# Performance work log

Measured on AMD Instinct MI355X. Metric: run time of the kernel, lower is better.

## Reference

```python
import jax, jax.numpy as jnp
import numpy as np

B, N, DIM = 2, 2048, 1024
HEADS, DH, NUM_MEM = 8, 64, 4
EPS = 1e-5


def layer_norm(x, gamma):
    mu = x.mean(-1, keepdims=True)
    var = ((x - mu) ** 2).mean(-1, keepdims=True)
    return (x - mu) * jax.lax.rsqrt(var + EPS) * gamma


def setup_inputs() -> dict:
    key = jax.random.key(0)
    ks = jax.random.split(key, 7)
    x = jax.random.normal(ks[0], (B, N, DIM), jnp.float32)
    mask = jax.random.randint(ks[1], (B, N), 0, 2) > 0
    attn_bias = jax.random.normal(ks[2], (HEADS, N, N), jnp.float32) * 0.02
    gamma = jnp.ones((DIM,), jnp.float32)
    Wq = jax.random.normal(ks[3], (DIM, HEADS * DH), jnp.float32) * (DIM ** -0.5)
    Wkv = jax.random.normal(ks[4], (DIM, 2 * DH), jnp.float32) * (DIM ** -0.5)
    mem_kv = jax.random.normal(ks[5], (2, NUM_MEM, DH), jnp.float32)
    Wout = jax.random.normal(ks[6], (HEADS * DH, DIM), jnp.float32) * ((HEADS * DH) ** -0.5)
    return dict(x=x, attn_bias=attn_bias, gamma=gamma, Wq=Wq, Wkv=Wkv,
                mem_kv=mem_kv, Wout=Wout, mask=mask)


def reference(x, attn_bias, gamma, Wq, Wkv, mem_kv, Wout, mask):
    b, n, _ = x.shape
    # norm applied to query path only; kv comes from pre-norm x (self-attention)
    xn = layer_norm(x, gamma)
    q = (xn @ Wq).reshape(b, n, HEADS, DH).transpose(0, 2, 1, 3) * (DH ** -0.5)  # b h n d
    kv = x @ Wkv  # multi-query: single shared kv head
    k, v = kv[..., :DH], kv[..., DH:]
    mk = jnp.broadcast_to(mem_kv[0], (b, NUM_MEM, DH))
    mv = jnp.broadcast_to(mem_kv[1], (b, NUM_MEM, DH))
    k = jnp.concatenate([mk, k], axis=1)  # b (m+n) d
    v = jnp.concatenate([mv, v], axis=1)
    j = n + NUM_MEM
    bias = jnp.pad(attn_bias, ((0, 0), (0, 0), (NUM_MEM, 0)))  # zero bias on mem tokens
    maskp = jnp.pad(mask, ((0, 0), (NUM_MEM, 0)), constant_values=True)
    sim = jnp.einsum('bhid,bjd->bhij', q, k) + bias
    neg = -jnp.finfo(sim.dtype).max
    sim = jnp.where(maskp[:, None, None, :], sim, neg)
    causal = jnp.triu(jnp.ones((n, j), bool), k=NUM_MEM + 1)  # mem tokens always visible
    sim = jnp.where(causal, neg, sim)
    attn = jax.nn.softmax(sim, axis=-1)
    out = jnp.einsum('bhij,bjd->bhid', attn, v)
    out = out.transpose(0, 2, 1, 3).reshape(b, n, HEADS * DH)
    return out @ Wout
```

## Files before the change

### kernel.cpp

```cpp
#include <hip/hip_runtime.h>
#include <hip/hip_bf16.h>
#include <float.h>

#define B_ 2
#define N_ 2048
#define DIM_ 1024
#define HEADS_ 8
#define DH_ 64
#define NUM_MEM_ 4
#define ROWS_ (B_ * N_)
#define QCOLS_ (HEADS_ * DH_)
#define JTOT_ (N_ + NUM_MEM_)
#define JPAD_ 2176
#define CHUNKS_PER_BH_ 77

typedef __attribute__((ext_vector_type(8))) short short8v;
typedef __attribute__((ext_vector_type(4))) float f32x4;

static __device__ __forceinline__ ushort f2b(float f) {
    __hip_bfloat16 hb = __float2bfloat16(f);
    return *(ushort*)&hb;
}
static __device__ __forceinline__ uint pk2(float a, float b) {
    return ((uint)f2b(b) << 16) | (uint)f2b(a);
}
static __device__ __forceinline__ float b2f_lo(uint u) {
    union { uint x; float f; } c; c.x = u << 16; return c.f;
}
static __device__ __forceinline__ float b2f_hi(uint u) {
    union { uint x; float f; } c; c.x = u & 0xffff0000u; return c.f;
}

__global__ __launch_bounds__(256) void ln_cast_kernel(const float* __restrict__ x,
                                                      const float* __restrict__ gamma,
                                                      ushort* __restrict__ xb,
                                                      ushort* __restrict__ xnb) {
    int row = blockIdx.x;
    const float4 v = ((const float4*)(x + (size_t)row * DIM_))[threadIdx.x];
    float s  = v.x + v.y + v.z + v.w;
    float s2 = v.x * v.x + v.y * v.y + v.z * v.z + v.w * v.w;
    #pragma unroll
    for (int off = 32; off > 0; off >>= 1) {
        s  += __shfl_down(s, off);
        s2 += __shfl_down(s2, off);
    }
    __shared__ float ws1[4], ws2[4];
    int lane = threadIdx.x & 63, wid = threadIdx.x >> 6;
    if (lane == 0) { ws1[wid] = s; ws2[wid] = s2; }
    __syncthreads();
    float tot  = ws1[0] + ws1[1] + ws1[2] + ws1[3];
    float tot2 = ws2[0] + ws2[1] + ws2[2] + ws2[3];
    float mu  = tot * (1.0f / DIM_);
    float var = tot2 * (1.0f / DIM_) - mu * mu;
    float rs  = rsqrtf(var + 1e-5f);
    const float4 g = ((const float4*)gamma)[threadIdx.x];
    float vv[4] = {v.x, v.y, v.z, v.w};
    float gg[4] = {g.x, g.y, g.z, g.w};
    ushort xo[4], xno[4];
    #pragma unroll
    for (int j = 0; j < 4; ++j) {
        xo[j]  = f2b(vv[j]);
        xno[j] = f2b((vv[j] - mu) * rs * gg[j]);
    }
    *(int2*)(xb  + (size_t)row * DIM_ + threadIdx.x * 4) = *(int2*)xo;
    *(int2*)(xnb + (size_t)row * DIM_ + threadIdx.x * 4) = *(int2*)xno;
}

static __device__ __forceinline__ void wtrans_body(const float* __restrict__ W,
                                                   ushort* __restrict__ Wt,
                                                   int K, int N, int t) {
    int n = t % N;
    int k0 = (t / N) * 8;
    ushort u[8];
    #pragma unroll
    for (int j = 0; j < 8; ++j) u[j] = f2b(W[(size_t)(k0 + j) * N + n]);
    *(int4*)(Wt + (size_t)n * K + k0) = *(int4*)u;
}

__global__ __launch_bounds__(256) void prep_kernel(const float* __restrict__ Wq,
                                                   const float* __restrict__ Wkv,
                                                   const float* __restrict__ Wout,
                                                   const float* __restrict__ mem_kv,
                                                   const int* __restrict__ mask,
                                                   ushort* __restrict__ Wqt,
                                                   ushort* __restrict__ Wkvt,
                                                   ushort* __restrict__ Woutt,
                                                   ushort* __restrict__ Kb,
                                                   ushort* __restrict__ Vt,
                                                   ushort* __restrict__ amask) {
    int bid = blockIdx.x;
    int tid = threadIdx.x;
    if (bid < 256) {
        wtrans_body(Wq, Wqt, DIM_, QCOLS_, bid * 256 + tid);
    } else if (bid < 320) {
        wtrans_body(Wkv, Wkvt, DIM_, 2 * DH_, (bid - 256) * 256 + tid);
    } else if (bid < 576) {
        wtrans_body(Wout, Woutt, QCOLS_, DIM_, (bid - 320) * 256 + tid);
    } else if (bid < 640) {
        int t = (bid - 576) * 256 + tid;
        int d  = t & 63;
        int ji = (t >> 6) & 127;
        int b  = t >> 13;
        int j  = (ji < NUM_MEM_) ? ji : (2048 + ji);
        float kv_ = 0.f, vv = 0.f;
        if (ji < NUM_MEM_) {
            kv_ = mem_kv[ji * DH_ + d];
            vv  = mem_kv[NUM_MEM_ * DH_ + ji * DH_ + d];
        }
        Kb[((size_t)(b * JPAD_) + j) * DH_ + d] = f2b(kv_);
        Vt[((size_t)(b * DH_) + d) * JPAD_ + j] = f2b(vv);
    } else {
        int t = (bid - 640) * 256 + tid;
        if (t < B_ * JPAD_) {
            int b = t / JPAD_;
            int j = t % JPAD_;
            float v;
            if (j < NUM_MEM_) v = 0.f;
            else if (j < JTOT_) v = mask[b * N_ + (j - NUM_MEM_)] ? 0.f : -1e30f;
            else v = -1e30f;
            amask[(size_t)b * JPAD_ + j] = f2b(v);
        }
    }
}

template<int MODE, int BM>
__global__ __launch_bounds__(256) void gemm_bf16(const ushort* __restrict__ A,
                                                 const ushort* __restrict__ Bt,
                                                 void* __restrict__ C,
                                                 void* __restrict__ C2,
                                                 int M, int N, int K) {
    constexpr int RT = BM / 64;
    __shared__ ushort As[BM][40];
    __shared__ ushort Bs[64][40];
    int tid = threadIdx.x;
    int w = tid >> 6, l = tid & 63, lg = l >> 4, ll = l & 15;
    int r0 = blockIdx.y * BM, c0 = blockIdx.x * 64;

    int arow = tid >> 2;
    int achk = (tid & 3) * 8;
    const ushort* Ap  = A + (size_t)(r0 + arow) * K + achk;
    const ushort* Ap2 = Ap + (size_t)64 * K;
    const ushort* Bp  = Bt + (size_t)(c0 + arow) * K + achk;

    int4 a0 = *(const int4*)Ap;
    int4 a1;
    if constexpr (RT == 2) a1 = *(const int4*)Ap2;
    int4 b0 = *(const int4*)Bp;

    f32x4 acc[RT][4] = {};

    int nk = K / 32;
    for (int ks = 0; ks < nk; ++ks) {
        __syncthreads();
        *(int4*)&As[arow][achk] = a0;
        if constexpr (RT == 2) *(int4*)&As[arow + 64][achk] = a1;
        *(int4*)&Bs[arow][achk] = b0;
        __syncthreads();
        int kn = (ks + 1 < nk) ? (ks + 1) * 32 : 0;
        a0 = *(const int4*)(Ap + kn);
        if constexpr (RT == 2) a1 = *(const int4*)(Ap2 + kn);
        b0 = *(const int4*)(Bp + kn);
        short8v af[RT], bf[4];
        #pragma unroll
        for (int rt = 0; rt < RT; ++rt)
            af[rt] = *(const short8v*)&As[w * 16 * RT + rt * 16 + ll][lg * 8];
        #pragma unroll
        for (int ct = 0; ct < 4; ++ct)
            bf[ct] = *(const short8v*)&Bs[ct * 16 + ll][lg * 8];
        __builtin_amdgcn_s_setprio(1);
        #pragma unroll
        for (int rt = 0; rt < RT; ++rt)
            #pragma unroll
            for (int ct = 0; ct < 4; ++ct)
                acc[rt][ct] = __builtin_amdgcn_mfma_f32_16x16x32_bf16(af[rt], bf[ct], acc[rt][ct], 0, 0, 0);
        __builtin_amdgcn_s_setprio(0);
    }

    #pragma unroll
    for (int rt = 0; rt < RT; ++rt) {
        #pragma unroll
        for (int ct = 0; ct < 4; ++ct) {
            #pragma unroll
            for (int r = 0; r < 4; ++r) {
                int row = r0 + w * 16 * RT + rt * 16 + lg * 4 + r;
                int col = c0 + ct * 16 + ll;
                float val = acc[rt][ct][r];
                if (MODE == 0) {
                    ((ushort*)C)[(size_t)row * QCOLS_ + col] = f2b(val * 0.125f);
                } else if (MODE == 1) {
                    int b = row >> 11;
                    int j = (row & 2047) + NUM_MEM_;
                    if (col < DH_)
                        ((ushort*)C)[((size_t)(b * JPAD_) + j) * DH_ + col] = f2b(val);
                    else
                        ((ushort*)C2)[((size_t)(b * DH_) + (col - DH_)) * JPAD_ + j] = f2b(val);
                } else {
                    ((float*)C)[(size_t)row * DIM_ + col] = val;
                }
            }
        }
    }
}

__global__ __launch_bounds__(256, 4) void fattn_split_kernel(const ushort* __restrict__ qb,
                                                             const ushort* __restrict__ Kb,
                                                             const ushort* __restrict__ Vt,
                                                             const float* __restrict__ bias,
                                                             const ushort* __restrict__ amask,
                                                             float* __restrict__ part_O,
                                                             float* __restrict__ part_ml) {
    __shared__ ushort Ks[64][72];
    __shared__ ushort Vs[64][72];
    __shared__ ushort Pt[4][16][72];

    int cid = blockIdx.x;
    int bh  = cid / CHUNKS_PER_BH_;
    int rem = cid - bh * CHUNKS_PER_BH_;
    int b = bh >> 3, h = bh & 7;
    int qt = 0, ci = 0;
    {
        int cum = 0;
        #pragma unroll 1
        for (int t = 0; t < 32; ++t) {
            int c = (t + 10) / 9;
            if (rem < cum + c) { qt = t; ci = rem - cum; break; }
            cum += c;
        }
    }
    int nt = qt + 2;
    int nc = (qt + 10) / 9;
    int t0 = ci * nt / nc;
    int t1 = (ci + 1) * nt / nc;
    int q0 = qt * 64;

    int tid = threadIdx.x;
    int w  = tid >> 6;
    int l  = tid & 63;
    int lg = l >> 4;
    int ll = l & 15;
    int i_row = q0 + w * 16 + ll;

    short8v aq0, aq1;
    {
        const ushort* qp = qb + ((size_t)(b * N_ + i_row)) * QCOLS_ + h * DH_;
        aq0 = *(const short8v*)(qp + lg * 8);
        aq1 = *(const short8v*)(qp + 32 + lg * 8);
    }

    const float*  bias_row = bias + ((size_t)h * N_ + i_row) * N_;
    const ushort* am_row   = amask + (size_t)b * JPAD_;

    int sr = tid >> 3, sc = (tid & 7) * 8;
    const ushort* KbB = Kb + (size_t)b * JPAD_ * DH_;
    const ushort* VtB = Vt + (size_t)b * DH_ * JPAD_;

    int jp0 = t0 * 64;
    int4 kr0 = *(const int4*)(KbB + (size_t)(jp0 + sr) * DH_ + sc);
    int4 kr1 = *(const int4*)(KbB + (size_t)(jp0 + sr + 32) * DH_ + sc);
    int4 vr0 = *(const int4*)(VtB + (size_t)sr * JPAD_ + jp0 + sc);
    int4 vr1 = *(const int4*)(VtB + (size_t)(sr + 32) * JPAD_ + jp0 + sc);

    f32x4 oacc[4] = {};
    float mrow1 = -1e30f, lsum1 = 0.f;

    for (int jt = t0; jt < t1; ++jt) {
        int j0 = jt * 64;
        __syncthreads();
        *(int4*)&Ks[sr][sc]      = kr0;
        *(int4*)&Ks[sr + 32][sc] = kr1;
        *(int4*)&Vs[sr][sc]      = vr0;
        *(int4*)&Vs[sr + 32][sc] = vr1;
        __syncthreads();

        float4 bb[4];
        uint2  am[4];
        #pragma unroll
        for (int ct = 0; ct < 4; ++ct) {
            int js = j0 + ct * 16 + lg * 4;
            int sj = js - NUM_MEM_;
            int sjc = sj < 0 ? 0 : (sj > N_ - 4 ? N_ - 4 : sj);
            bb[ct] = *(const float4*)(bias_row + sjc);
            am[ct] = *(const uint2*)(am_row + js);
        }

        int jn0 = (jt + 1 < t1 ? jt + 1 : jt) * 64;
        kr0 = *(const int4*)(KbB + (size_t)(jn0 + sr) * DH_ + sc);
        kr1 = *(const int4*)(KbB + (size_t)(jn0 + sr + 32) * DH_ + sc);
        vr0 = *(const int4*)(VtB + (size_t)sr * JPAD_ + jn0 + sc);
        vr1 = *(const int4*)(VtB + (size_t)(sr + 32) * JPAD_ + jn0 + sc);

        float s[4][4];
        #pragma unroll
        for (int ct = 0; ct < 4; ++ct) {
            f32x4 acc = {};
            short8v bk0 = *(const short8v*)&Ks[ct * 16 + ll][lg * 8];
            short8v bk1 = *(const short8v*)&Ks[ct * 16 + ll][32 + lg * 8];
            __builtin_amdgcn_s_setprio(1);
            acc = __builtin_amdgcn_mfma_f32_16x16x32_bf16(bk0, aq0, acc, 0, 0, 0);
            acc = __builtin_amdgcn_mfma_f32_16x16x32_bf16(bk1, aq1, acc, 0, 0, 0);
            __builtin_amdgcn_s_setprio(0);
            float amf[4] = { b2f_lo(am[ct].x), b2f_hi(am[ct].x),
                             b2f_lo(am[ct].y), b2f_hi(am[ct].y) };
            #pragma unroll
            for (int r = 0; r < 4; ++r)
                s[ct][r] = acc[r] + bb[ct][r] + amf[r];
            if (ct == 0 && jt == 0) {
                #pragma unroll
                for (int r = 0; r < 4; ++r)
                    if (lg == 0) s[0][r] = acc[r];
            }
        }
        if (jt >= qt) {
            #pragma unroll
            for (int ct = 0; ct < 4; ++ct)
                #pragma unroll
                for (int r = 0; r < 4; ++r) {
                    int js = j0 + ct * 16 + lg * 4 + r;
                    s[ct][r] = (js <= i_row + NUM_MEM_) ? s[ct][r] : -1e30f;
                }
        }

        float m01 = fmaxf(fmaxf(s[0][0], s[0][1]), fmaxf(s[0][2], s[0][3]));
        float m23 = fmaxf(fmaxf(s[1][0], s[1][1]), fmaxf(s[1][2], s[1][3]));
        float m45 = fmaxf(fmaxf(s[2][0], s[2][1]), fmaxf(s[2][2], s[2][3]));
        float m67 = fmaxf(fmaxf(s[3][0], s[3][1]), fmaxf(s[3][2], s[3][3]));
        float m = fmaxf(fmaxf(m01, m23), fmaxf(m45, m67));
        m = fmaxf(m, __shfl_xor(m, 16));
        m = fmaxf(m, __shfl_xor(m, 32));
        float mn = fmaxf(mrow1, m);
        float scl = __expf(mrow1 - mn);
        mrow1 = mn;

        float ps = 0.f;
        #pragma unroll
        for (int ct = 0; ct < 4; ++ct)
            #pragma unroll
            for (int r = 0; r < 4; ++r) {
                float p = __expf(s[ct][r] - mn);
                s[ct][r] = p;
                ps += p;
            }
        ps += __shfl_xor(ps, 16);
        ps += __shfl_xor(ps, 32);
        lsum1 = lsum1 * scl + ps;

        #pragma unroll
        for (int ct = 0; ct < 4; ++ct) {
            uint2 pu;
            pu.x = pk2(s[ct][0], s[ct][1]);
            pu.y = pk2(s[ct][2], s[ct][3]);
            *(uint2*)&Pt[w][ll][ct * 16 + lg * 4] = pu;
        }
        #pragma unroll
        for (int dt = 0; dt < 4; ++dt)
            #pragma unroll
            for (int r = 0; r < 4; ++r) oacc[dt][r] *= scl;

        #pragma unroll
        for (int c = 0; c < 2; ++c) {
            short8v ptf = *(const short8v*)&Pt[w][ll][c * 32 + lg * 8];
            __builtin_amdgcn_s_setprio(1);
            #pragma unroll
            for (int dt = 0; dt < 4; ++dt) {
                short8v bv = *(const short8v*)&Vs[dt * 16 + ll][c * 32 + lg * 8];
                oacc[dt] = __builtin_amdgcn_mfma_f32_16x16x32_bf16(bv, ptf, oacc[dt], 0, 0, 0);
            }
            __builtin_amdgcn_s_setprio(0);
        }
    }

    int slot = (bh * 32 + qt) * 4 + ci;
    float* po = part_O + (size_t)slot * 4096;
    #pragma unroll
    for (int dt = 0; dt < 4; ++dt)
        *(f32x4*)&po[(w * 16 + ll) * 64 + dt * 16 + lg * 4] = oacc[dt];
    if (lg == 0) {
        part_ml[(size_t)slot * 128 + (w * 16 + ll) * 2]     = mrow1;
        part_ml[(size_t)slot * 128 + (w * 16 + ll) * 2 + 1] = lsum1;
    }
}

__global__ __launch_bounds__(256) void merge_kernel(const float* __restrict__ part_O,
                                                    const float* __restrict__ part_ml,
                                                    ushort* __restrict__ attn_ob) {
    int bid = blockIdx.x;
    int qt = bid & 31;
    int bh = bid >> 5;
    int b = bh >> 3, h = bh & 7;
    int nc = (qt + 10) / 9;
    int tid = threadIdx.x;
    int row = tid >> 2;
    int dseg = (tid & 3) * 16;
    int slot0 = bid * 4;

    float M = -1e30f;
    #pragma unroll
    for (int c = 0; c < 4; ++c) {
        if (c >= nc) break;
        M = fmaxf(M, part_ml[(size_t)(slot0 + c) * 128 + row * 2]);
    }
    float den = 0.f;
    float num[16] = {};
    #pragma unroll
    for (int c = 0; c < 4; ++c) {
        if (c >= nc) break;
        float m_c = part_ml[(size_t)(slot0 + c) * 128 + row * 2];
        float l_c = part_ml[(size_t)(slot0 + c) * 128 + row * 2 + 1];
        float wgt = __expf(m_c - M);
        den += wgt * l_c;
        const float4* src = (const float4*)(part_O + (size_t)(slot0 + c) * 4096 + row * 64 + dseg);
        #pragma unroll
        for (int e = 0; e < 4; ++e) {
            float4 v = src[e];
            num[e * 4 + 0] += wgt * v.x;
            num[e * 4 + 1] += wgt * v.y;
            num[e * 4 + 2] += wgt * v.z;
            num[e * 4 + 3] += wgt * v.w;
        }
    }
    float inv = 1.f / den;
    ushort o[16];
    #pragma unroll
    for (int e = 0; e < 16; ++e) o[e] = f2b(num[e] * inv);
    int i = qt * 64 + row;
    ushort* dst = attn_ob + ((size_t)(b * N_ + i)) * QCOLS_ + h * DH_ + dseg;
    *(int4*)dst = *(int4*)o;
    *(int4*)(dst + 8) = *(int4*)(o + 8);
}

extern "C" void kernel_launch(void* const* d_in, const int* in_sizes, int n_in,
                              void* d_out, int out_size, void* d_ws, size_t ws_size,
                              hipStream_t stream) {
    const float* x         = (const float*)d_in[0];
    const float* attn_bias = (const float*)d_in[1];
    const float* gamma     = (const float*)d_in[2];
    const float* Wq        = (const float*)d_in[3];
    const float* Wkv       = (const float*)d_in[4];
    const float* mem_kv    = (const float*)d_in[5];
    const float* Wout      = (const float*)d_in[6];
    const int*   mask      = (const int*)d_in[7];
    float* out = (float*)d_out;

    char* wsb = (char*)d_ws;
    ushort* xb      = (ushort*)wsb;
    ushort* xnb     = (ushort*)(wsb + (8u  << 20));
    ushort* qb      = (ushort*)(wsb + (16u << 20));
    ushort* attn_ob = (ushort*)(wsb + (20u << 20));
    ushort* Kb      = (ushort*)(wsb + (24u << 20));
    ushort* Vt      = (ushort*)(wsb + (25u << 20));
    ushort* Wqt     = (ushort*)(wsb + (26u << 20));
    ushort* Wkvt    = (ushort*)(wsb + (27u << 20));
    ushort* Woutt   = (ushort*)(wsb + (28u << 20));
    ushort* amask   = (ushort*)(wsb + (29u << 20));
    float*  part_O  = (float*)(wsb + (32u << 20));
    float*  part_ml = (float*)(wsb + (64u << 20));

    ln_cast_kernel<<<ROWS_, 256, 0, stream>>>(x, gamma, xb, xnb);
    prep_kernel<<<657, 256, 0, stream>>>(Wq, Wkv, Wout, mem_kv, mask, Wqt, Wkvt, Woutt, Kb, Vt, amask);

    gemm_bf16<0, 64><<<dim3(QCOLS_ / 64, ROWS_ / 64), 256, 0, stream>>>(xnb, Wqt, qb, nullptr, ROWS_, QCOLS_, DIM_);
    gemm_bf16<1, 64><<<dim3((2 * DH_) / 64, ROWS_ / 64), 256, 0, stream>>>(xb, Wkvt, Kb, Vt, ROWS_, 2 * DH_, DIM_);
    fattn_split_kernel<<<16 * CHUNKS_PER_BH_, 256, 0, stream>>>(qb, Kb, Vt, attn_bias, amask, part_O, part_ml);
    merge_kernel<<<512, 256, 0, stream>>>(part_O, part_ml, attn_ob);
    gemm_bf16<2, 128><<<dim3(DIM_ / 64, ROWS_ / 128), 256, 0, stream>>>(attn_ob, Woutt, out, nullptr, ROWS_, DIM_, QCOLS_);
}
```

Before: 108.2 us.

## Process both batches per attention block to share attn_bias loads

Each attention block now handles one head for both batch elements, so the per-head attn_bias tile (fp32, the largest input) is read once and used for both batches instead of once per batch. K/V tiles for both batches are staged in doubled shared memory, with per-batch softmax state and accumulators. The grid halves to 616 blocks and launch bounds drop to 3 blocks per CU to fit the higher register and LDS use, which cuts parallelism and occupancy.

```diff
diff --git a/kernel.cpp b/kernel.cpp
--- a/kernel.cpp
+++ b/kernel.cpp
@@ -202,21 +202,20 @@
     }
 }
 
-__global__ __launch_bounds__(256, 4) void fattn_split_kernel(const ushort* __restrict__ qb,
+__global__ __launch_bounds__(256, 3) void fattn_split_kernel(const ushort* __restrict__ qb,
                                                              const ushort* __restrict__ Kb,
                                                              const ushort* __restrict__ Vt,
                                                              const float* __restrict__ bias,
                                                              const ushort* __restrict__ amask,
                                                              float* __restrict__ part_O,
                                                              float* __restrict__ part_ml) {
-    __shared__ ushort Ks[64][72];
-    __shared__ ushort Vs[64][72];
+    __shared__ ushort Ks[2][64][72];
+    __shared__ ushort Vs[2][64][72];
     __shared__ ushort Pt[4][16][72];
 
     int cid = blockIdx.x;
-    int bh  = cid / CHUNKS_PER_BH_;
-    int rem = cid - bh * CHUNKS_PER_BH_;
-    int b = bh >> 3, h = bh & 7;
+    int h   = cid / CHUNKS_PER_BH_;
+    int rem = cid - h * CHUNKS_PER_BH_;
     int qt = 0, ci = 0;
     {
         int cum = 0;
@@ -240,143 +239,163 @@
     int ll = l & 15;
     int i_row = q0 + w * 16 + ll;
 
-    short8v aq0, aq1;
-    {
+    short8v aq0[2], aq1[2];
+    #pragma unroll
+    for (int b = 0; b < 2; ++b) {
         const ushort* qp = qb + ((size_t)(b * N_ + i_row)) * QCOLS_ + h * DH_;
-        aq0 = *(const short8v*)(qp + lg * 8);
-        aq1 = *(const short8v*)(qp + 32 + lg * 8);
-    }
-
-    const float*  bias_row = bias + ((size_t)h * N_ + i_row) * N_;
-    const ushort* am_row   = amask + (size_t)b * JPAD_;
+        aq0[b] = *(const short8v*)(qp + lg * 8);
+        aq1[b] = *(const short8v*)(qp + 32 + lg * 8);
+    }
+
+    const float* bias_row = bias + ((size_t)h * N_ + i_row) * N_;
 
     int sr = tid >> 3, sc = (tid & 7) * 8;
-    const ushort* KbB = Kb + (size_t)b * JPAD_ * DH_;
-    const ushort* VtB = Vt + (size_t)b * DH_ * JPAD_;
+    const ushort* KbB[2] = { Kb, Kb + (size_t)JPAD_ * DH_ };
+    const ushort* VtB[2] = { Vt, Vt + (size_t)DH_ * JPAD_ };
 
     int jp0 = t0 * 64;
-    int4 kr0 = *(const int4*)(KbB + (size_t)(jp0 + sr) * DH_ + sc);
-    int4 kr1 = *(const int4*)(KbB + (size_t)(jp0 + sr + 32) * DH_ + sc);
-    int4 vr0 = *(const int4*)(VtB + (size_t)sr * JPAD_ + jp0 + sc);
-    int4 vr1 = *(const int4*)(VtB + (size_t)(sr + 32) * JPAD_ + jp0 + sc);
-
-    f32x4 oacc[4] = {};
-    float mrow1 = -1e30f, lsum1 = 0.f;
+    int4 kr[2][2], vr[2][2];
+    #pragma unroll
+    for (int b = 0; b < 2; ++b) {
+        kr[b][0] = *(const int4*)(KbB[b] + (size_t)(jp0 + sr) * DH_ + sc);
+        kr[b][1] = *(const int4*)(KbB[b] + (size_t)(jp0 + sr + 32) * DH_ + sc);
+        vr[b][0] = *(const int4*)(VtB[b] + (size_t)sr * JPAD_ + jp0 + sc);
+        vr[b][1] = *(const int4*)(VtB[b] + (size_t)(sr + 32) * JPAD_ + jp0 + sc);
+    }
+
+    f32x4 oacc[2][4] = {};
+    float mrow[2] = {-1e30f, -1e30f}, lsum[2] = {0.f, 0.f};
 
     for (int jt = t0; jt < t1; ++jt) {
         int j0 = jt * 64;
-        __syncthreads();
-        *(int4*)&Ks[sr][sc]      = kr0;
-        *(int4*)&Ks[sr + 32][sc] = kr1;
-        *(int4*)&Vs[sr][sc]      = vr0;
-        *(int4*)&Vs[sr + 32][sc] = vr1;
-        __syncthreads();
 
         float4 bb[4];
-        uint2  am[4];
         #pragma unroll
         for (int ct = 0; ct < 4; ++ct) {
             int js = j0 + ct * 16 + lg * 4;
             int sj = js - NUM_MEM_;
             int sjc = sj < 0 ? 0 : (sj > N_ - 4 ? N_ - 4 : sj);
             bb[ct] = *(const float4*)(bias_row + sjc);
-            am[ct] = *(const uint2*)(am_row + js);
-        }
+        }
+
+        __syncthreads();
+        #pragma unroll
+        for (int b = 0; b < 2; ++b) {
+            *(int4*)&Ks[b][sr][sc]      = kr[b][0];
+            *(int4*)&Ks[b][sr + 32][sc] = kr[b][1];
+            *(int4*)&Vs[b][sr][sc]      = vr[b][0];
+            *(int4*)&Vs[b][sr + 32][sc] = vr[b][1];
+        }
+        __syncthreads();
 
         int jn0 = (jt + 1 < t1 ? jt + 1 : jt) * 64;
-        kr0 = *(const int4*)(KbB + (size_t)(jn0 + sr) * DH_ + sc);
-        kr1 = *(const int4*)(KbB + (size_t)(jn0 + sr + 32) * DH_ + sc);
-        vr0 = *(const int4*)(VtB + (size_t)sr * JPAD_ + jn0 + sc);
-        vr1 = *(const int4*)(VtB + (size_t)(sr + 32) * JPAD_ + jn0 + sc);
-
-        float s[4][4];
-        #pragma unroll
-        for (int ct = 0; ct < 4; ++ct) {
-            f32x4 acc = {};
-            short8v bk0 = *(const short8v*)&Ks[ct * 16 + ll][lg * 8];
-            short8v bk1 = *(const short8v*)&Ks[ct * 16 + ll][32 + lg * 8];
-            __builtin_amdgcn_s_setprio(1);
-            acc = __builtin_amdgcn_mfma_f32_16x16x32_bf16(bk0, aq0, acc, 0, 0, 0);
-            acc = __builtin_amdgcn_mfma_f32_16x16x32_bf16(bk1, aq1, acc, 0, 0, 0);
-            __builtin_amdgcn_s_setprio(0);
-            float amf[4] = { b2f_lo(am[ct].x), b2f_hi(am[ct].x),
-                             b2f_lo(am[ct].y), b2f_hi(am[ct].y) };
-            #pragma unroll
-            for (int r = 0; r < 4; ++r)
-                s[ct][r] = acc[r] + bb[ct][r] + amf[r];
-            if (ct == 0 && jt == 0) {
+        #pragma unroll
+        for (int b = 0; b < 2; ++b) {
+            kr[b][0] = *(const int4*)(KbB[b] + (size_t)(jn0 + sr) * DH_ + sc);
+            kr[b][1] = *(const int4*)(KbB[b] + (size_t)(jn0 + sr + 32) * DH_ + sc);
+            vr[b][0] = *(const int4*)(VtB[b] + (size_t)sr * JPAD_ + jn0 + sc);
+            vr[b][1] = *(const int4*)(VtB[b] + (size_t)(sr + 32) * JPAD_ + jn0 + sc);
+        }
+
+        #pragma unroll
+        for (int b = 0; b < 2; ++b) {
+            uint2 am[4];
+            #pragma unroll
+            for (int ct = 0; ct < 4; ++ct)
+                am[ct] = *(const uint2*)(amask + (size_t)b * JPAD_ + j0 + ct * 16 + lg * 4);
+
+            float s[4][4];
+            #pragma unroll
+            for (int ct = 0; ct < 4; ++ct) {
+                f32x4 acc = {};
+                short8v bk0 = *(const short8v*)&Ks[b][ct * 16 + ll][lg * 8];
+                short8v bk1 = *(const short8v*)&Ks[b][ct * 16 + ll][32 + lg * 8];
+                __builtin_amdgcn_s_setprio(1);
+                acc = __builtin_amdgcn_mfma_f32_16x16x32_bf16(bk0, aq0[b], acc, 0, 0, 0);
+                acc = __builtin_amdgcn_mfma_f32_16x16x32_bf16(bk1, aq1[b], acc, 0, 0, 0);
+                __builtin_amdgcn_s_setprio(0);
+                float amf[4] = { b2f_lo(am[ct].x), b2f_hi(am[ct].x),
+                                 b2f_lo(am[ct].y), b2f_hi(am[ct].y) };
                 #pragma unroll
                 for (int r = 0; r < 4; ++r)
-                    if (lg == 0) s[0][r] = acc[r];
+                    s[ct][r] = acc[r] + bb[ct][r] + amf[r];
+                if (ct == 0 && jt == 0) {
+                    #pragma unroll
+                    for (int r = 0; r < 4; ++r)
+                        if (lg == 0) s[0][r] = acc[r];
+                }
             }
-        }
-        if (jt >= qt) {
+            if (jt >= qt) {
+                #pragma unroll
+                for (int ct = 0; ct < 4; ++ct)
+                    #pragma unroll
+                    for (int r = 0; r < 4; ++r) {
+                        int js = j0 + ct * 16 + lg * 4 + r;
+                        s[ct][r] = (js <= i_row + NUM_MEM_) ? s[ct][r] : -1e30f;
+                    }
+            }
+
+            float m01 = fmaxf(fmaxf(s[0][0], s[0][1]), fmaxf(s[0][2], s[0][3]));
+            float m23 = fmaxf(fmaxf(s[1][0], s[1][1]), fmaxf(s[1][2], s[1][3]));
+            float m45 = fmaxf(fmaxf(s[2][0], s[2][1]), fmaxf(s[2][2], s[2][3]));
+            float m67 = fmaxf(fmaxf(s[3][0], s[3][1]), fmaxf(s[3][2], s[3][3]));
+            float m = fmaxf(fmaxf(m01, m23), fmaxf(m45, m67));
+            m = fmaxf(m, __shfl_xor(m, 16));
+            m = fmaxf(m, __shfl_xor(m, 32));
+            float mn = fmaxf(mrow[b], m);
+            float scl = __expf(mrow[b] - mn);
+            mrow[b] = mn;
+
+            float ps = 0.f;
             #pragma unroll
             for (int ct = 0; ct < 4; ++ct)
                 #pragma unroll
                 for (int r = 0; r < 4; ++r) {
-                    int js = j0 + ct * 16 + lg * 4 + r;
-                    s[ct][r] = (js <= i_row + NUM_MEM_) ? s[ct][r] : -1e30f;
+                    float p = __expf(s[ct][r] - mn);
+                    s[ct][r] = p;
+                    ps += p;
                 }
-        }
-
-        float m01 = fmaxf(fmaxf(s[0][0], s[0][1]), fmaxf(s[0][2], s[0][3]));
-        float m23 = fmaxf(fmaxf(s[1][0], s[1][1]), fmaxf(s[1][2], s[1][3]));
-        float m45 = fmaxf(fmaxf(s[2][0], s[2][1]), fmaxf(s[2][2], s[2][3]));
-        float m67 = fmaxf(fmaxf(s[3][0], s[3][1]), fmaxf(s[3][2], s[3][3]));
-        float m = fmaxf(fmaxf(m01, m23), fmaxf(m45, m67));
-        m = fmaxf(m, __shfl_xor(m, 16));
-        m = fmaxf(m, __shfl_xor(m, 32));
-        float mn = fmaxf(mrow1, m);
-        float scl = __expf(mrow1 - mn);
-        mrow1 = mn;
-
-        float ps = 0.f;
-        #pragma unroll
-        for (int ct = 0; ct < 4; ++ct)
-            #pragma unroll
-            for (int r = 0; r < 4; ++r) {
-                float p = __expf(s[ct][r] - mn);
-                s[ct][r] = p;
-                ps += p;
+            ps += __shfl_xor(ps, 16);
+            ps += __shfl_xor(ps, 32);
+            lsum[b] = lsum[b] * scl + ps;
+
+            #pragma unroll
+            for (int ct = 0; ct < 4; ++ct) {
+                uint2 pu;
+                pu.x = pk2(s[ct][0], s[ct][1]);
+                pu.y = pk2(s[ct][2], s[ct][3]);
+                *(uint2*)&Pt[w][ll][ct * 16 + lg * 4] = pu;
             }
-        ps += __shfl_xor(ps, 16);
-        ps += __shfl_xor(ps, 32);
-        lsum1 = lsum1 * scl + ps;
-
-        #pragma unroll
-        for (int ct = 0; ct < 4; ++ct) {
-            uint2 pu;
-            pu.x = pk2(s[ct][0], s[ct][1]);
-            pu.y = pk2(s[ct][2], s[ct][3]);
-            *(uint2*)&Pt[w][ll][ct * 16 + lg * 4] = pu;
-        }
+            #pragma unroll
+            for (int dt = 0; dt < 4; ++dt)
+                #pragma unroll
+                for (int r = 0; r < 4; ++r) oacc[b][dt][r] *= scl;
+
+            #pragma unroll
+            for (int c = 0; c < 2; ++c) {
+                short8v ptf = *(const short8v*)&Pt[w][ll][c * 32 + lg * 8];
+                __builtin_amdgcn_s_setprio(1);
+                #pragma unroll
+                for (int dt = 0; dt < 4; ++dt) {
+                    short8v bv = *(const short8v*)&Vs[b][dt * 16 + ll][c * 32 + lg * 8];
+                    oacc[b][dt] = __builtin_amdgcn_mfma_f32_16x16x32_bf16(bv, ptf, oacc[b][dt], 0, 0, 0);
+                }
+                __builtin_amdgcn_s_setprio(0);
+            }
+        }
+    }
+
+    #pragma unroll
+    for (int b = 0; b < 2; ++b) {
+        int slot = (((b * 8 + h) * 32) + qt) * 4 + ci;
+        float* po = part_O + (size_t)slot * 4096;
         #pragma unroll
         for (int dt = 0; dt < 4; ++dt)
-            #pragma unroll
-            for (int r = 0; r < 4; ++r) oacc[dt][r] *= scl;
-
-        #pragma unroll
-        for (int c = 0; c < 2; ++c) {
-            short8v ptf = *(const short8v*)&Pt[w][ll][c * 32 + lg * 8];
-            __builtin_amdgcn_s_setprio(1);
-            #pragma unroll
-            for (int dt = 0; dt < 4; ++dt) {
-                short8v bv = *(const short8v*)&Vs[dt * 16 + ll][c * 32 + lg * 8];
-                oacc[dt] = __builtin_amdgcn_mfma_f32_16x16x32_bf16(bv, ptf, oacc[dt], 0, 0, 0);
-            }
-            __builtin_amdgcn_s_setprio(0);
-        }
-    }
-
-    int slot = (bh * 32 + qt) * 4 + ci;
-    float* po = part_O + (size_t)slot * 4096;
-    #pragma unroll
-    for (int dt = 0; dt < 4; ++dt)
-        *(f32x4*)&po[(w * 16 + ll) * 64 + dt * 16 + lg * 4] = oacc[dt];
-    if (lg == 0) {
-        part_ml[(size_t)slot * 128 + (w * 16 + ll) * 2]     = mrow1;
-        part_ml[(size_t)slot * 128 + (w * 16 + ll) * 2 + 1] = lsum1;
+            *(f32x4*)&po[(w * 16 + ll) * 64 + dt * 16 + lg * 4] = oacc[b][dt];
+        if (lg == 0) {
+            part_ml[(size_t)slot * 128 + (w * 16 + ll) * 2]     = mrow[b];
+            part_ml[(size_t)slot * 128 + (w * 16 + ll) * 2 + 1] = lsum[b];
+        }
     }
 }
 
@@ -460,7 +479,7 @@
 
     gemm_bf16<0, 64><<<dim3(QCOLS_ / 64, ROWS_ / 64), 256, 0, stream>>>(xnb, Wqt, qb, nullptr, ROWS_, QCOLS_, DIM_);
     gemm_bf16<1, 64><<<dim3((2 * DH_) / 64, ROWS_ / 64), 256, 0, stream>>>(xb, Wkvt, Kb, Vt, ROWS_, 2 * DH_, DIM_);
-    fattn_split_kernel<<<16 * CHUNKS_PER_BH_, 256, 0, stream>>>(qb, Kb, Vt, attn_bias, amask, part_O, part_ml);
+    fattn_split_kernel<<<HEADS_ * CHUNKS_PER_BH_, 256, 0, stream>>>(qb, Kb, Vt, attn_bias, amask, part_O, part_ml);
     merge_kernel<<<512, 256, 0, stream>>>(part_O, part_ml, attn_ob);
     gemm_bf16<2, 128><<<dim3(DIM_ / 64, ROWS_ / 128), 256, 0, stream>>>(attn_ob, Woutt, out, nullptr, ROWS_, DIM_, QCOLS_);
 }
```

New measurement: 164.2 us. +51.7%, slower.
